# Optimization experiments

Measured on AMD Instinct MI355X. Metric: run time of the kernel, lower is better.

## Reference

```python
import jax, jax.numpy as jnp
import numpy as np

D = 768          # embedding_dim
H = 8            # attention heads
DH = D // H
HID = 512        # hidden_dim
N_LAYERS = 3     # graph conv layers
N_ETYPES = 5
LN_EPS = 1e-5


def setup_inputs() -> dict:
    key = jax.random.key(0)
    ks = jax.random.split(key, 32)
    N, E = 4096, 131072
    s = lambda fan: 1.0 / np.sqrt(fan)
    inp = {
        'node_features': jax.random.normal(ks[0], (N, D), jnp.float32),
        'edge_indices': jax.random.randint(ks[1], (2, E), 0, N, jnp.int64),
        'edge_types': jax.random.randint(ks[2], (E,), 0, N_ETYPES, jnp.int64),
        'node_types': jax.random.randint(ks[3], (N,), 0, 3, jnp.int64),
        # embedding tables
        'statute_emb': jax.random.normal(ks[4], (1000, D), jnp.float32),
        'case_emb': jax.random.normal(ks[5], (5000, D), jnp.float32),
        'article_emb': jax.random.normal(ks[6], (2000, D), jnp.float32),
        # per-layer conv params (stacked over 3 layers)
        'conv_msg_W': jax.random.uniform(ks[7], (N_LAYERS, N_ETYPES, D, D), jnp.float32, -s(D), s(D)),
        'conv_msg_b': jax.random.uniform(ks[8], (N_LAYERS, N_ETYPES, D), jnp.float32, -s(D), s(D)),
        'conv_upd_W': jax.random.uniform(ks[9], (N_LAYERS, D, 2 * D), jnp.float32, -s(2 * D), s(2 * D)),
        'conv_upd_b': jax.random.uniform(ks[10], (N_LAYERS, D), jnp.float32, -s(2 * D), s(2 * D)),
        'conv_ln_g': jnp.ones((N_LAYERS, D), jnp.float32),
        'conv_ln_b': jnp.zeros((N_LAYERS, D), jnp.float32),
        # MultiheadAttention params
        'in_proj_W': jax.random.uniform(ks[11], (3 * D, D), jnp.float32, -s(D), s(D)),
        'in_proj_b': jnp.zeros((3 * D,), jnp.float32),
        'out_proj_W': jax.random.uniform(ks[12], (D, D), jnp.float32, -s(D), s(D)),
        'out_proj_b': jnp.zeros((D,), jnp.float32),
        # network analyzer MLP
        'an_W1': jax.random.uniform(ks[13], (HID, D), jnp.float32, -s(D), s(D)),
        'an_b1': jax.random.uniform(ks[14], (HID,), jnp.float32, -s(D), s(D)),
        'an_W2': jax.random.uniform(ks[15], (HID // 2, HID), jnp.float32, -s(HID), s(HID)),
        'an_b2': jax.random.uniform(ks[16], (HID // 2,), jnp.float32, -s(HID), s(HID)),
        'an_W3': jax.random.uniform(ks[17], (1, HID // 2), jnp.float32, -s(HID // 2), s(HID // 2)),
        'an_b3': jax.random.uniform(ks[18], (1,), jnp.float32, -s(HID // 2), s(HID // 2)),
    }
    return inp


def _layer_norm(h, g, b):
    mu = h.mean(-1, keepdims=True)
    var = ((h - mu) ** 2).mean(-1, keepdims=True)
    return g * (h - mu) / jnp.sqrt(var + LN_EPS) + b


def _conv_layer(x, msg_W, msg_b, upd_W, upd_b, ln_g, ln_b, src, tgt, etypes):
    # x: [N, D]; src/tgt: [E]; etypes: [E]
    src_feats = x[src]                               # gather [E, D]
    agg = jnp.zeros_like(x)
    for t in range(N_ETYPES):                        # small fixed loop over edge types
        mask = (etypes == t)[:, None]
        msgs = jnp.where(mask, src_feats @ msg_W[t].T + msg_b[t], 0.0)
        agg = agg + jax.ops.segment_sum(msgs, tgt, num_segments=x.shape[0])
    combined = jnp.concatenate([x, agg], axis=-1)    # [N, 2D]
    upd = jax.nn.relu(combined @ upd_W.T + upd_b)    # dropout is identity in eval
    return _layer_norm(x + upd, ln_g, ln_b)


def reference(node_features, edge_indices, edge_types, node_types,
              statute_emb, case_emb, article_emb,
              conv_msg_W, conv_msg_b, conv_upd_W, conv_upd_b, conv_ln_g, conv_ln_b,
              in_proj_W, in_proj_b, out_proj_W, out_proj_b,
              an_W1, an_b1, an_W2, an_b2, an_W3, an_b3):
    N = node_features.shape[0]
    idx = jnp.arange(N)
    # per-node-type embedding lookup (i % table_size), vectorized
    emb = jnp.where((node_types == 0)[:, None], statute_emb[idx % 1000],
          jnp.where((node_types == 1)[:, None], case_emb[idx % 5000],
                    article_emb[idx % 2000]))
    x = node_features + emb

    src, tgt = edge_indices[0], edge_indices[1]
    for l in range(N_LAYERS):
        x = _conv_layer(x, conv_msg_W[l], conv_msg_b[l], conv_upd_W[l], conv_upd_b[l],
                        conv_ln_g[l], conv_ln_b[l], src, tgt, edge_types)

    # self-attention over all nodes (batch of 1), torch MHA semantics, eval mode
    qkv = x @ in_proj_W.T + in_proj_b                # [N, 3D]
    q, k, v = jnp.split(qkv, 3, axis=-1)
    to_h = lambda t: t.reshape(N, H, DH).transpose(1, 0, 2)   # [H, N, DH]
    q, k, v = to_h(q), to_h(k), to_h(v)
    scores = jnp.einsum('hqd,hkd->hqk', q, k) / jnp.sqrt(jnp.float32(DH))
    attn = jax.nn.softmax(scores, axis=-1)           # [H, N, N]
    ctx = jnp.einsum('hqk,hkd->hqd', attn, v).transpose(1, 0, 2).reshape(N, D)
    graph_repr = ctx @ out_proj_W.T + out_proj_b     # [N, D]
    attn_weights = attn.mean(0)                      # averaged over heads [N, N]

    pooled = graph_repr.mean(axis=0)                 # [D]
    h = jax.nn.relu(pooled @ an_W1.T + an_b1)
    h = jax.nn.relu(h @ an_W2.T + an_b2)
    network_score = jax.nn.sigmoid(h @ an_W3.T + an_b3)

    return x, graph_repr, network_score, attn_weights
```

## Files before the change

### kernel.cpp

```cpp
#include <hip/hip_runtime.h>

typedef unsigned short u16;
typedef unsigned int u32;
typedef __attribute__((ext_vector_type(4))) float f32x4;
typedef __attribute__((ext_vector_type(8))) __bf16 bf16x8;
typedef __attribute__((ext_vector_type(4))) unsigned int u32x4;

#define DEV static __device__ __forceinline__

#define NNODE 4096
#define DMODEL 768
#define NEDGE 131072

static constexpr size_t OFF_X     = 0;
static constexpr size_t OFF_X2    = 12582912;
static constexpr size_t OFF_AMSG  = 25165824;
static constexpr size_t OFF_AUPD  = 31457280;
static constexpr size_t OFF_WMSG  = 44040192;
static constexpr size_t OFF_WUPD  = 61734912;
static constexpr size_t OFF_WIP   = 68812800;
static constexpr size_t OFF_WOP   = 72351744;
static constexpr size_t OFF_Q     = 73531392;
static constexpr size_t OFF_K     = 79822848;
static constexpr size_t OFF_V     = 86114304;
static constexpr size_t OFF_CTX   = 92405760;
static constexpr size_t OFF_STATS = 98697216;
static constexpr size_t OFF_ML    = 98959360;
static constexpr size_t OFF_DEG   = 100007936;
static constexpr size_t OFF_OFFS  = 100024320;
static constexpr size_t OFF_CUR   = 100040960;
static constexpr size_t OFF_PACK  = 100057344;
static constexpr size_t OFF_PART  = 100581632;
static constexpr size_t OFF_POOL  = 100778240;
static constexpr size_t OFF_H1    = 100781312;
static constexpr size_t OFF_H2    = 100783360;
static constexpr size_t WS_TOTAL  = 100784384;

__device__ __attribute__((aligned(256))) unsigned char g_ws[WS_TOTAL];

DEV u16 f2bf(float f) {
  return __builtin_bit_cast(u16, (__bf16)f);
}
DEV void gl_lds16(const void* g, void* l) {
  __builtin_amdgcn_global_load_lds((const __attribute__((address_space(1))) void*)g,
                                   (__attribute__((address_space(3))) void*)l, 16, 0, 0);
}
DEV f32x4 mfma16(bf16x8 a, bf16x8 b, f32x4 c) {
  return __builtin_amdgcn_mfma_f32_16x16x32_bf16(a, b, c, 0, 0, 0);
}

__global__ void zero_kernel(int* p, int n) {
  int i = blockIdx.x * 256 + threadIdx.x;
  if (i < n) p[i] = 0;
}
__global__ void deg_kernel(const int* __restrict__ ei, int* __restrict__ deg) {
  int e = blockIdx.x * 256 + threadIdx.x;
  atomicAdd(&deg[ei[NEDGE + e]], 1);
}
__global__ void scan_kernel(const int* __restrict__ deg, int* __restrict__ offs, int* __restrict__ cur) {
  __shared__ int buf[1024];
  int t = threadIdx.x;
  int v0 = deg[t*4], v1 = deg[t*4+1], v2 = deg[t*4+2], v3 = deg[t*4+3];
  int s = v0 + v1 + v2 + v3;
  buf[t] = s;
  __syncthreads();
  for (int off = 1; off < 1024; off <<= 1) {
    int add = (t >= off) ? buf[t - off] : 0;
    __syncthreads();
    buf[t] += add;
    __syncthreads();
  }
  int run = buf[t] - s;
  offs[t*4] = run; cur[t*4] = run; run += v0;
  offs[t*4+1] = run; cur[t*4+1] = run; run += v1;
  offs[t*4+2] = run; cur[t*4+2] = run; run += v2;
  offs[t*4+3] = run; cur[t*4+3] = run; run += v3;
  if (t == 1023) offs[4096] = run;
}
__global__ void scatter_kernel(const int* __restrict__ ei, const int* __restrict__ ety,
                               int* __restrict__ cur, int* __restrict__ pack) {
  int e = blockIdx.x * 256 + threadIdx.x;
  int tg = ei[NEDGE + e];
  int pos = atomicAdd(&cur[tg], 1);
  pack[pos] = ei[e] | (ety[e] << 12);
}

__global__ void convert_bf_kernel(const float* __restrict__ W, u16* __restrict__ out, int total) {
  for (int i = blockIdx.x * 256 + threadIdx.x; i < total; i += gridDim.x * 256)
    out[i] = f2bf(W[i]);
}

__global__ void embed_kernel(const float* __restrict__ nf, const int* __restrict__ nty,
                             const float* __restrict__ se, const float* __restrict__ ce,
                             const float* __restrict__ ae,
                             float* __restrict__ x, u16* __restrict__ Amsg, u16* __restrict__ Aupd) {
  int v = blockIdx.x, t = threadIdx.x;
  int typ = nty[v];
  const float* tab = (typ == 0) ? se + (size_t)(v % 1000) * 768
                   : (typ == 1) ? ce + (size_t)(v % 5000) * 768
                                : ae + (size_t)(v % 2000) * 768;
  #pragma unroll
  for (int i = 0; i < 3; ++i) {
    int c = t + i * 256;
    float f = nf[(size_t)v * 768 + c] + tab[c];
    x[(size_t)v * 768 + c] = f;
    u16 hi = f2bf(f);
    Amsg[(size_t)v * 768 + c] = hi;
    Aupd[(size_t)v * 1536 + c] = hi;
  }
}

template<int EPI>
__global__ void __launch_bounds__(256, 3)
gemm_bt(const u16* __restrict__ A, int lda,
        const u16* __restrict__ B0, int ldb, int K,
        const float* __restrict__ bias0,
        float* __restrict__ C0, int ldc,
        const float* __restrict__ resid,
        u16* __restrict__ oq, u16* __restrict__ okk, u16* __restrict__ ov,
        long zsB, int zsBias, long zsC)
{
  __shared__ alignas(16) u16 sA[8192];
  __shared__ alignas(16) u16 sB[8192];
  const int tid = threadIdx.x;
  const int lane = tid & 63, wid = tid >> 6;
  const int wr = wid >> 1, wc = wid & 1;
  const int li = lane & 15, g = lane >> 4;
  const int bm = blockIdx.y * 128, bn = blockIdx.x * 128;
  const int z = blockIdx.z;
  const u16* B = B0 + (size_t)z * zsB;
  const float* bias = bias0 + (size_t)z * zsBias;

  const int srow = tid >> 3;
  const int scol = ((tid & 7) ^ (srow & 7)) * 8;
  const u16* Ag = A + (size_t)(bm + srow) * lda + scol;
  const u16* Bg = B + (size_t)(bn + srow) * ldb + scol;
  char* sAw = (char*)sA + wid * 1024;
  char* sBw = (char*)sB + wid * 1024;

  f32x4 acc[4][4];
  const f32x4 vz = {0.f, 0.f, 0.f, 0.f};
  #pragma unroll
  for (int i = 0; i < 4; ++i)
    #pragma unroll
    for (int j = 0; j < 4; ++j) acc[i][j] = vz;

  for (int k0 = 0; k0 < K; k0 += 64) {
    __syncthreads();
    #pragma unroll
    for (int is = 0; is < 4; ++is) {
      gl_lds16(Ag + (size_t)is * 32 * lda + k0, sAw + is * 4096);
      gl_lds16(Bg + (size_t)is * 32 * ldb + k0, sBw + is * 4096);
    }
    __syncthreads();
    #pragma unroll
    for (int kc = 0; kc < 2; ++kc) {
      bf16x8 av[4], bv[4];
      #pragma unroll
      for (int mt = 0; mt < 4; ++mt) {
        int row = wr * 64 + mt * 16 + li;
        av[mt] = *(const bf16x8*)((const char*)sA + row * 128 + ((kc * 64 + g * 16) ^ ((row & 7) << 4)));
      }
      #pragma unroll
      for (int nt = 0; nt < 4; ++nt) {
        int row = wc * 64 + nt * 16 + li;
        bv[nt] = *(const bf16x8*)((const char*)sB + row * 128 + ((kc * 64 + g * 16) ^ ((row & 7) << 4)));
      }
      #pragma unroll
      for (int mt = 0; mt < 4; ++mt)
        #pragma unroll
        for (int nt = 0; nt < 4; ++nt)
          acc[mt][nt] = mfma16(av[mt], bv[nt], acc[mt][nt]);
    }
  }
  #pragma unroll
  for (int mt = 0; mt < 4; ++mt) {
    #pragma unroll
    for (int nt = 0; nt < 4; ++nt) {
      #pragma unroll
      for (int r = 0; r < 4; ++r) {
        int gr = bm + wr * 64 + mt * 16 + g * 4 + r;
        int gc = bn + wc * 64 + nt * 16 + li;
        float v = acc[mt][nt][r] + bias[gc];
        if (EPI == 0) {
          C0[(size_t)z * zsC + (size_t)gr * ldc + gc] = v;
        } else if (EPI == 1) {
          C0[(size_t)gr * ldc + gc] = fmaxf(v, 0.f) + resid[(size_t)gr * 768 + gc];
        } else {
          int part = gc / 768;
          int j = gc - part * 768;
          int h = j / 96, d = j - h * 96;
          if (part == 0)      oq[((size_t)(h << 12) + gr) * 96 + d] = f2bf(v * (float)(0.10206207261596575 * 1.4426950408889634));
          else if (part == 1) okk[((size_t)(h << 12) + gr) * 96 + d] = f2bf(v);
          else                ov[((size_t)h * 96 + d) * 4096 + gr] = f2bf(v);
        }
      }
    }
  }
}

__global__ void agg_kernel(const float* __restrict__ Y, const int* __restrict__ offs,
                           const int* __restrict__ pack, u16* __restrict__ Aupd) {
  const int v = blockIdx.x, t = threadIdx.x;
  float a0 = 0.f, a1 = 0.f, a2 = 0.f;
  const int beg = offs[v], end = offs[v + 1];
  for (int i = beg; i < end; ++i) {
    int p = pack[i];
    const float* row = Y + (size_t)p * 768;
    a0 += row[t]; a1 += row[t + 256]; a2 += row[t + 512];
  }
  size_t b = (size_t)v * 1536 + 768;
  Aupd[b + t] = f2bf(a0); Aupd[b + t + 256] = f2bf(a1); Aupd[b + t + 512] = f2bf(a2);
}

__global__ void ln_kernel(const float* __restrict__ xin, const float* __restrict__ gam,
                          const float* __restrict__ bet,
                          float* __restrict__ x, u16* __restrict__ Amsg, u16* __restrict__ Aupd,
                          float* __restrict__ xcopy) {
  __shared__ float red[256];
  int v = blockIdx.x, t = threadIdx.x;
  const float* r = xin + (size_t)v * 768;
  float v0 = r[t], v1 = r[t + 256], v2 = r[t + 512];
  red[t] = v0 + v1 + v2;
  __syncthreads();
  for (int off = 128; off > 0; off >>= 1) { if (t < off) red[t] += red[t + off]; __syncthreads(); }
  float mu = red[0] * (1.f / 768.f);
  __syncthreads();
  float d0 = v0 - mu, d1 = v1 - mu, d2 = v2 - mu;
  red[t] = d0 * d0 + d1 * d1 + d2 * d2;
  __syncthreads();
  for (int off = 128; off > 0; off >>= 1) { if (t < off) red[t] += red[t + off]; __syncthreads(); }
  float rstd = rsqrtf(red[0] * (1.f / 768.f) + 1e-5f);
  float dv[3] = {d0, d1, d2};
  #pragma unroll
  for (int i = 0; i < 3; ++i) {
    int c = t + i * 256;
    float y = gam[c] * dv[i] * rstd + bet[c];
    x[(size_t)v * 768 + c] = y;
    if (xcopy) xcopy[(size_t)v * 768 + c] = y;
    u16 hi = f2bf(y);
    Amsg[(size_t)v * 768 + c] = hi;
    Aupd[(size_t)v * 1536 + c] = hi;
  }
}

__global__ void __launch_bounds__(256, 3)
flash_kernel(const u16* __restrict__ Qb, const u16* __restrict__ Kb,
             const u16* __restrict__ Vtb, float* __restrict__ Op,
             float* __restrict__ Mp, float* __restrict__ Lp) {
  __shared__ alignas(16) u16 sK[6144];
  __shared__ alignas(16) u16 sV[6144];
  __shared__ alignas(16) u16 sP[4][2048];
  const int tid = threadIdx.x, lane = tid & 63, wid = tid >> 6;
  const int li = lane & 15, g = lane >> 4;
  const int qt = blockIdx.x, h = blockIdx.y, kcb = blockIdx.z;
  const int vrow = tid >> 3, vcol = (tid & 7) ^ (vrow & 7);

  const u16* Qg = Qb + ((size_t)(h << 12) + qt * 128 + wid * 32 + li) * 96 + g * 8;
  bf16x8 aq0[3], aq1[3];
  #pragma unroll
  for (int kc = 0; kc < 3; ++kc) {
    aq0[kc] = *(const bf16x8*)(Qg + kc * 32);
    aq1[kc] = *(const bf16x8*)(Qg + 1536 + kc * 32);
  }

  float m0 = -1e30f, l0 = 0.f, m1 = -1e30f, l1 = 0.f;
  const f32x4 vz = {0.f, 0.f, 0.f, 0.f};
  f32x4 o0[6], o1[6];
  #pragma unroll
  for (int dt = 0; dt < 6; ++dt) { o0[dt] = vz; o1[dt] = vz; }

  const char* Kg = (const char*)(Kb + (size_t)(h << 12) * 96);
  const char* Vg = (const char*)(Vtb + (size_t)h * 96 * 4096);
  char* sKb = (char*)sK; char* sVb = (char*)sV; char* sPb = (char*)sP[wid];

  for (int kt = kcb * 16; kt < kcb * 16 + 16; ++kt) {
    __syncthreads();
    #pragma unroll
    for (int j = 0; j < 3; ++j) {
      gl_lds16(Kg + ((size_t)(kt * 64 + lane) * 96 + j * 32 + wid * 8) * 2, sKb + j * 4096 + wid * 1024);
      gl_lds16(Vg + (size_t)(j * 32 + vrow) * 8192 + kt * 128 + vcol * 16, sVb + j * 4096 + wid * 1024);
    }
    __syncthreads();

    f32x4 s0[4], s1[4];
    __builtin_amdgcn_s_setprio(1);
    #pragma unroll
    for (int nt = 0; nt < 4; ++nt) {
      s0[nt] = vz; s1[nt] = vz;
      #pragma unroll
      for (int kc = 0; kc < 3; ++kc) {
        bf16x8 bk = *(const bf16x8*)(sKb + kc * 4096 + g * 1024 + (nt * 16 + li) * 16);
        s0[nt] = mfma16(bk, aq0[kc], s0[nt]);
        s1[nt] = mfma16(bk, aq1[kc], s1[nt]);
      }
    }
    __builtin_amdgcn_s_setprio(0);

    {
      float mx = fmaxf(fmaxf(fmaxf(s0[0][0], s0[0][1]), fmaxf(s0[0][2], s0[0][3])),
                       fmaxf(fmaxf(s0[1][0], s0[1][1]), fmaxf(s0[1][2], s0[1][3])));
      mx = fmaxf(mx, fmaxf(fmaxf(fmaxf(s0[2][0], s0[2][1]), fmaxf(s0[2][2], s0[2][3])),
                           fmaxf(fmaxf(s0[3][0], s0[3][1]), fmaxf(s0[3][2], s0[3][3]))));
      mx = fmaxf(mx, __shfl_xor(mx, 16));
      mx = fmaxf(mx, __shfl_xor(mx, 32));
      if (__any(mx > m0 + 8.f)) {
        float mnew = fmaxf(m0, mx);
        float alpha = exp2f(m0 - mnew);
        l0 *= alpha;
        #pragma unroll
        for (int dt = 0; dt < 6; ++dt) o0[dt] *= alpha;
        m0 = mnew;
      }
      float rs = 0.f;
      #pragma unroll
      for (int nt = 0; nt < 4; ++nt)
        #pragma unroll
        for (int r = 0; r < 4; ++r) { float p = exp2f(s0[nt][r] - m0); s0[nt][r] = p; rs += p; }
      rs += __shfl_xor(rs, 16);
      rs += __shfl_xor(rs, 32);
      l0 += rs;
      #pragma unroll
      for (int nt = 0; nt < 4; ++nt)
        #pragma unroll
        for (int r0 = 0; r0 < 4; r0 += 2) {
          u32 w = (u32)f2bf(s0[nt][r0]) | ((u32)f2bf(s0[nt][r0 + 1]) << 16);
          *(u32*)(sPb + li * 128 + (((nt * 16 + g * 4 + r0) * 2) ^ ((li & 7) << 4))) = w;
        }
    }
    {
      float mx = fmaxf(fmaxf(fmaxf(s1[0][0], s1[0][1]), fmaxf(s1[0][2], s1[0][3])),
                       fmaxf(fmaxf(s1[1][0], s1[1][1]), fmaxf(s1[1][2], s1[1][3])));
      mx = fmaxf(mx, fmaxf(fmaxf(fmaxf(s1[2][0], s1[2][1]), fmaxf(s1[2][2], s1[2][3])),
                           fmaxf(fmaxf(s1[3][0], s1[3][1]), fmaxf(s1[3][2], s1[3][3]))));
      mx = fmaxf(mx, __shfl_xor(mx, 16));
      mx = fmaxf(mx, __shfl_xor(mx, 32));
      if (__any(mx > m1 + 8.f)) {
        float mnew = fmaxf(m1, mx);
        float alpha = exp2f(m1 - mnew);
        l1 *= alpha;
        #pragma unroll
        for (int dt = 0; dt < 6; ++dt) o1[dt] *= alpha;
        m1 = mnew;
      }
      float rs = 0.f;
      #pragma unroll
      for (int nt = 0; nt < 4; ++nt)
        #pragma unroll
        for (int r = 0; r < 4; ++r) { float p = exp2f(s1[nt][r] - m1); s1[nt][r] = p; rs += p; }
      rs += __shfl_xor(rs, 16);
      rs += __shfl_xor(rs, 32);
      l1 += rs;
      #pragma unroll
      for (int nt = 0; nt < 4; ++nt)
        #pragma unroll
        for (int r0 = 0; r0 < 4; r0 += 2) {
          u32 w = (u32)f2bf(s1[nt][r0]) | ((u32)f2bf(s1[nt][r0 + 1]) << 16);
          *(u32*)(sPb + (16 + li) * 128 + (((nt * 16 + g * 4 + r0) * 2) ^ ((li & 7) << 4))) = w;
        }
    }

    __builtin_amdgcn_s_setprio(1);
    #pragma unroll
    for (int kc2 = 0; kc2 < 2; ++kc2) {
      bf16x8 pa0 = *(const bf16x8*)(sPb + li * 128 + ((kc2 * 64 + g * 16) ^ ((li & 7) << 4)));
      bf16x8 pa1 = *(const bf16x8*)(sPb + (16 + li) * 128 + ((kc2 * 64 + g * 16) ^ ((li & 7) << 4)));
      #pragma unroll
      for (int dt = 0; dt < 6; ++dt) {
        int d = dt * 16 + li;
        bf16x8 bvv = *(const bf16x8*)(sVb + d * 128 + ((kc2 * 64 + g * 16) ^ ((d & 7) << 4)));
        o0[dt] = mfma16(pa0, bvv, o0[dt]);
        o1[dt] = mfma16(pa1, bvv, o1[dt]);
      }
    }
    __builtin_amdgcn_s_setprio(0);
  }
  int bq = qt * 128 + wid * 32;
  size_t cb = (size_t)(((kcb * 8 + h) << 12));
  #pragma unroll
  for (int dt = 0; dt < 6; ++dt)
    #pragma unroll
    for (int r = 0; r < 4; ++r) {
      int d = dt * 16 + li;
      Op[(cb + bq + g * 4 + r) * 96 + d] = o0[dt][r];
      Op[(cb + bq + 16 + g * 4 + r) * 96 + d] = o1[dt][r];
    }
  if (g == 0) {
    Mp[cb + bq + li] = m0;      Lp[cb + bq + li] = l0;
    Mp[cb + bq + 16 + li] = m1; Lp[cb + bq + 16 + li] = l1;
  }
}

__global__ void merge_kernel(const float* __restrict__ Op, const float* __restrict__ Mp,
                             const float* __restrict__ Lp,
                             u16* __restrict__ ctxb, float* __restrict__ stats) {
  int row = blockIdx.x, t = threadIdx.x;
  #pragma unroll
  for (int i = 0; i < 3; ++i) {
    int idx = t + i * 256;
    int h = idx / 96, d = idx - h * 96;
    int base = (h << 12) + row;
    float m0 = Mp[base], m1 = Mp[32768 + base], m2 = Mp[65536 + base], m3 = Mp[98304 + base];
    float M = fmaxf(fmaxf(m0, m1), fmaxf(m2, m3));
    float w0 = exp2f(m0 - M), w1 = exp2f(m1 - M), w2 = exp2f(m2 - M), w3 = exp2f(m3 - M);
    float L = w0 * Lp[base] + w1 * Lp[32768 + base] + w2 * Lp[65536 + base] + w3 * Lp[98304 + base];
    float o = w0 * Op[(size_t)base * 96 + d]
            + w1 * Op[(size_t)(32768 + base) * 96 + d]
            + w2 * Op[(size_t)(65536 + base) * 96 + d]
            + w3 * Op[(size_t)(98304 + base) * 96 + d];
    float invl = 1.f / L;
    ctxb[(size_t)row * 768 + idx] = f2bf(o * invl);
    if (d == 0) {
      stats[base] = M;
      stats[32768 + base] = invl;
    }
  }
}

__global__ void __launch_bounds__(256, 3)
mean_kernel(const u16* __restrict__ Qb, const u16* __restrict__ Kb,
            const float* __restrict__ stats, float* __restrict__ out) {
  __shared__ alignas(16) u16 sQ[12288];
  __shared__ alignas(16) u16 sK2[6144];
  const int tid = threadIdx.x, lane = tid & 63, wid = tid >> 6;
  const int li = lane & 15, g = lane >> 4;
  const int q0 = blockIdx.x * 128, k0 = blockIdx.y * 64;
  const f32x4 vz = {0.f, 0.f, 0.f, 0.f};
  f32x4 macc0[4], macc1[4];
  #pragma unroll
  for (int nt = 0; nt < 4; ++nt) { macc0[nt] = vz; macc1[nt] = vz; }
  char* sQb = (char*)sQ; char* sKb = (char*)sK2;
  const int rq = (wid & 1) * 64 + lane;
  const int ccb = wid >> 1;

  for (int h = 0; h < 8; ++h) {
    __syncthreads();
    #pragma unroll
    for (int i = 0; i < 6; ++i) {
      int cc = i * 2 + ccb, kc = cc >> 2, gg = cc & 3;
      gl_lds16((const char*)Qb + ((size_t)(h << 12) + q0 + rq) * 192 + kc * 64 + gg * 16,
               sQb + kc * 8192 + gg * 2048 + (wid & 1) * 1024);
    }
    #pragma unroll
    for (int i = 0; i < 3; ++i) {
      int c = i * 4 + wid, kc = c >> 2, gg = c & 3;
      gl_lds16((const char*)Kb + ((size_t)(h << 12) + k0 + lane) * 192 + kc * 64 + gg * 16,
               sKb + kc * 4096 + gg * 1024);
    }
    __syncthreads();

    bf16x8 a20[3], a21[3];
    #pragma unroll
    for (int kc = 0; kc < 3; ++kc) {
      a20[kc] = *(const bf16x8*)(sQb + kc * 8192 + g * 2048 + (wid * 32 + li) * 16);
      a21[kc] = *(const bf16x8*)(sQb + kc * 8192 + g * 2048 + (wid * 32 + 16 + li) * 16);
    }
    f32x4 s0[4], s1[4];
    __builtin_amdgcn_s_setprio(1);
    #pragma unroll
    for (int nt = 0; nt < 4; ++nt) {
      s0[nt] = vz; s1[nt] = vz;
      #pragma unroll
      for (int kc = 0; kc < 3; ++kc) {
        bf16x8 bk = *(const bf16x8*)(sKb + kc * 4096 + g * 1024 + (nt * 16 + li) * 16);
        s0[nt] = mfma16(a20[kc], bk, s0[nt]);
        s1[nt] = mfma16(a21[kc], bk, s1[nt]);
      }
    }
    __builtin_amdgcn_s_setprio(0);
    #pragma unroll
    for (int r = 0; r < 4; ++r) {
      int row0 = q0 + wid * 32 + g * 4 + r;
      float mm0 = stats[(h << 12) + row0];
      float si0 = 0.125f * stats[32768 + (h << 12) + row0];
      int row1 = row0 + 16;
      float mm1 = stats[(h << 12) + row1];
      float si1 = 0.125f * stats[32768 + (h << 12) + row1];
      #pragma unroll
      for (int nt = 0; nt < 4; ++nt) {
        macc0[nt][r] += exp2f(s0[nt][r] - mm0) * si0;
        macc1[nt][r] += exp2f(s1[nt][r] - mm1) * si1;
      }
    }
  }
  #pragma unroll
  for (int nt = 0; nt < 4; ++nt)
    #pragma unroll
    for (int r = 0; r < 4; ++r) {
      out[(size_t)(q0 + wid * 32 + g * 4 + r) * 4096 + k0 + nt * 16 + li] = macc0[nt][r];
      out[(size_t)(q0 + wid * 32 + 16 + g * 4 + r) * 4096 + k0 + nt * 16 + li] = macc1[nt][r];
    }
}

__global__ void colsum_kernel(const float* __restrict__ gr, float* __restrict__ part) {
  int b = blockIdx.x, t = threadIdx.x;
  float s0 = 0.f, s1 = 0.f, s2 = 0.f;
  for (int rr = 0; rr < 64; ++rr) {
    const float* row = gr + (size_t)(b * 64 + rr) * 768;
    s0 += row[t]; s1 += row[t + 256]; s2 += row[t + 512];
  }
  part[b * 768 + t] = s0; part[b * 768 + t + 256] = s1; part[b * 768 + t + 512] = s2;
}
__global__ void pool_kernel(const float* __restrict__ part, float* __restrict__ pool) {
  int t = blockIdx.x * 256 + threadIdx.x;
  float s = 0.f;
  #pragma unroll 8
  for (int b = 0; b < 64; ++b) s += part[b * 768 + t];
  pool[t] = s * (1.f / 4096.f);
}
template<int KDIM>
__global__ void mlp_fc_kernel(const float* __restrict__ in, const float* __restrict__ Wm,
                              const float* __restrict__ bb, float* __restrict__ outv) {
  int o = blockIdx.x * 4 + (threadIdx.x >> 6);
  int lane = threadIdx.x & 63;
  const float* w = Wm + (size_t)o * KDIM;
  float s = 0.f;
  #pragma unroll
  for (int k = lane; k < KDIM; k += 64) s += w[k] * in[k];
  s += __shfl_xor(s, 1);  s += __shfl_xor(s, 2);  s += __shfl_xor(s, 4);
  s += __shfl_xor(s, 8);  s += __shfl_xor(s, 16); s += __shfl_xor(s, 32);
  if (lane == 0) outv[o] = fmaxf(s + bb[o], 0.f);
}
__global__ void mlp3_kernel(const float* __restrict__ h2,
                            const float* __restrict__ W3, const float* __restrict__ b3,
                            float* __restrict__ out) {
  __shared__ float red[256];
  int t = threadIdx.x;
  red[t] = W3[t] * h2[t];
  __syncthreads();
  for (int off = 128; off > 0; off >>= 1) { if (t < off) red[t] += red[t + off]; __syncthreads(); }
  if (t == 0) out[0] = 1.f / (1.f + __expf(-(red[0] + b3[0])));
}

extern "C" void kernel_launch(void* const* d_in, const int* in_sizes, int n_in,
                              void* d_out, int out_size, void* d_ws, size_t ws_size,
                              hipStream_t stream) {
  const float* nf   = (const float*)d_in[0];
  const int*   ei   = (const int*)d_in[1];
  const int*   ety  = (const int*)d_in[2];
  const int*   nty  = (const int*)d_in[3];
  const float* se   = (const float*)d_in[4];
  const float* ce   = (const float*)d_in[5];
  const float* ae   = (const float*)d_in[6];
  const float* msgW = (const float*)d_in[7];
  const float* msgb = (const float*)d_in[8];
  const float* updW = (const float*)d_in[9];
  const float* updb = (const float*)d_in[10];
  const float* lng  = (const float*)d_in[11];
  const float* lnb  = (const float*)d_in[12];
  const float* ipW  = (const float*)d_in[13];
  const float* ipb  = (const float*)d_in[14];
  const float* opW  = (const float*)d_in[15];
  const float* opb  = (const float*)d_in[16];
  const float* aW1  = (const float*)d_in[17];
  const float* ab1  = (const float*)d_in[18];
  const float* aW2  = (const float*)d_in[19];
  const float* ab2  = (const float*)d_in[20];
  const float* aW3  = (const float*)d_in[21];
  const float* ab3  = (const float*)d_in[22];

  void* wsp = nullptr;
  hipGetSymbolAddress(&wsp, HIP_SYMBOL(g_ws));
  unsigned char* W = (unsigned char*)wsp;

  float* x     = (float*)(W + OFF_X);
  float* x2    = (float*)(W + OFF_X2);
  u16* Amsg    = (u16*)(W + OFF_AMSG);
  u16* Aupd    = (u16*)(W + OFF_AUPD);
  u16* Wmsg    = (u16*)(W + OFF_WMSG);
  u16* Wupd    = (u16*)(W + OFF_WUPD);
  u16* Wip     = (u16*)(W + OFF_WIP);
  u16* Wop     = (u16*)(W + OFF_WOP);
  u16* Qb      = (u16*)(W + OFF_Q);
  u16* Kb      = (u16*)(W + OFF_K);
  u16* Vtb     = (u16*)(W + OFF_V);
  u16* Ctxb    = (u16*)(W + OFF_CTX);
  float* stats = (float*)(W + OFF_STATS);
  float* Mp    = (float*)(W + OFF_ML);
  float* Lp    = Mp + 131072;
  int* deg     = (int*)(W + OFF_DEG);
  int* offs    = (int*)(W + OFF_OFFS);
  int* cur     = (int*)(W + OFF_CUR);
  int* pack    = (int*)(W + OFF_PACK);
  float* part  = (float*)(W + OFF_PART);
  float* pool  = (float*)(W + OFF_POOL);
  float* h1b   = (float*)(W + OFF_H1);
  float* h2b   = (float*)(W + OFF_H2);

  float* out_x    = (float*)d_out;
  float* out_gr   = out_x + (size_t)NNODE * DMODEL;
  float* out_sc   = out_gr + (size_t)NNODE * DMODEL;
  float* out_attn = out_sc + 1;
  float* Y        = out_attn;
  float* Op       = out_attn;

  zero_kernel<<<16, 256, 0, stream>>>(deg, NNODE);
  deg_kernel<<<NEDGE / 256, 256, 0, stream>>>(ei, deg);
  scan_kernel<<<1, 1024, 0, stream>>>(deg, offs, cur);
  scatter_kernel<<<NEDGE / 256, 256, 0, stream>>>(ei, ety, cur, pack);

  convert_bf_kernel<<<2048, 256, 0, stream>>>(msgW, Wmsg, 3 * 5 * 768 * 768);
  convert_bf_kernel<<<1024, 256, 0, stream>>>(updW, Wupd, 3 * 768 * 1536);
  convert_bf_kernel<<<1024, 256, 0, stream>>>(ipW, Wip, 2304 * 768);
  convert_bf_kernel<<<512, 256, 0, stream>>>(opW, Wop, 768 * 768);

  embed_kernel<<<NNODE, 256, 0, stream>>>(nf, nty, se, ce, ae, x, Amsg, Aupd);

  for (int l = 0; l < 3; ++l) {
    gemm_bt<0><<<dim3(6, 32, 5), 256, 0, stream>>>(Amsg, 768,
        Wmsg + (size_t)l * 5 * 768 * 768, 768, 768,
        msgb + (size_t)l * 5 * 768, Y, 768, nullptr, nullptr, nullptr, nullptr,
        (long)768 * 768, 768, (long)NNODE * DMODEL);
    agg_kernel<<<NNODE, 256, 0, stream>>>(Y, offs, pack, Aupd);
    gemm_bt<1><<<dim3(6, 32, 1), 256, 0, stream>>>(Aupd, 1536,
        Wupd + (size_t)l * 768 * 1536, 1536, 1536,
        updb + (size_t)l * 768, x2, 768, x, nullptr, nullptr, nullptr, 0, 0, 0);
    ln_kernel<<<NNODE, 256, 0, stream>>>(x2, lng + (size_t)l * 768, lnb + (size_t)l * 768,
        x, Amsg, Aupd, (l == 2) ? out_x : nullptr);
  }

  gemm_bt<2><<<dim3(18, 32, 1), 256, 0, stream>>>(Amsg, 768, Wip, 768, 768,
      ipb, nullptr, 0, nullptr, Qb, Kb, Vtb, 0, 0, 0);
  flash_kernel<<<dim3(32, 8, 4), 256, 0, stream>>>(Qb, Kb, Vtb, Op, Mp, Lp);
  merge_kernel<<<NNODE, 256, 0, stream>>>(Op, Mp, Lp, Ctxb, stats);
  mean_kernel<<<dim3(32, 64), 256, 0, stream>>>(Qb, Kb, stats, out_attn);
  gemm_bt<0><<<dim3(6, 32, 1), 256, 0, stream>>>(Ctxb, 768, Wop, 768, 768,
      opb, out_gr, 768, nullptr, nullptr, nullptr, nullptr, 0, 0, 0);

  colsum_kernel<<<64, 256, 0, stream>>>(out_gr, part);
  pool_kernel<<<3, 256, 0, stream>>>(part, pool);
  mlp_fc_kernel<768><<<128, 256, 0, stream>>>(pool, aW1, ab1, h1b);
  mlp_fc_kernel<512><<<64, 256, 0, stream>>>(h1b, aW2, ab2, h2b);
  mlp3_kernel<<<1, 256, 0, stream>>>(h2b, aW3, ab3, out_sc);
}
```

Baseline: 741.1 us.

## Load K/V fragments directly into registers with double-buffered K prefetch in flash kernel

Removes the shared-memory staging of K and V tiles and the two block-wide barriers per tile in the flash attention kernel. Each wave now loads its MFMA operand fragments for K and V straight from global memory into registers, and prefetches the next tile's K while the softmax runs, alternating between two register buffers. Launch bounds drop from 3 to 2 waves per SIMD to make room for the extra registers. In exchange, each wave loads K/V redundantly instead of sharing via LDS, so global/L2 traffic rises and occupancy falls.

```diff
diff --git a/kernel.cpp b/kernel.cpp
--- a/kernel.cpp
+++ b/kernel.cpp
@@ -244,17 +244,29 @@
   }
 }
 
-__global__ void __launch_bounds__(256, 3)
+DEV void kload(bf16x8* kk, const u16* Kg, int row0, int li, int g) {
+  #pragma unroll
+  for (int nt = 0; nt < 4; ++nt)
+    #pragma unroll
+    for (int kc = 0; kc < 3; ++kc)
+      kk[nt * 3 + kc] = *(const bf16x8*)(Kg + (size_t)(row0 + nt * 16 + li) * 96 + kc * 32 + g * 8);
+}
+DEV void vload(bf16x8* vv, const u16* Vg, int col0, int li, int g) {
+  #pragma unroll
+  for (int dt = 0; dt < 6; ++dt)
+    #pragma unroll
+    for (int kc2 = 0; kc2 < 2; ++kc2)
+      vv[dt * 2 + kc2] = *(const bf16x8*)(Vg + (size_t)(dt * 16 + li) * 4096 + col0 + kc2 * 32 + g * 8);
+}
+
+__global__ void __launch_bounds__(256, 2)
 flash_kernel(const u16* __restrict__ Qb, const u16* __restrict__ Kb,
              const u16* __restrict__ Vtb, float* __restrict__ Op,
              float* __restrict__ Mp, float* __restrict__ Lp) {
-  __shared__ alignas(16) u16 sK[6144];
-  __shared__ alignas(16) u16 sV[6144];
   __shared__ alignas(16) u16 sP[4][2048];
   const int tid = threadIdx.x, lane = tid & 63, wid = tid >> 6;
   const int li = lane & 15, g = lane >> 4;
   const int qt = blockIdx.x, h = blockIdx.y, kcb = blockIdx.z;
-  const int vrow = tid >> 3, vcol = (tid & 7) ^ (vrow & 7);
 
   const u16* Qg = Qb + ((size_t)(h << 12) + qt * 128 + wid * 32 + li) * 96 + g * 8;
   bf16x8 aq0[3], aq1[3];
@@ -270,111 +282,113 @@
   #pragma unroll
   for (int dt = 0; dt < 6; ++dt) { o0[dt] = vz; o1[dt] = vz; }
 
-  const char* Kg = (const char*)(Kb + (size_t)(h << 12) * 96);
-  const char* Vg = (const char*)(Vtb + (size_t)h * 96 * 4096);
-  char* sKb = (char*)sK; char* sVb = (char*)sV; char* sPb = (char*)sP[wid];
-
-  for (int kt = kcb * 16; kt < kcb * 16 + 16; ++kt) {
-    __syncthreads();
-    #pragma unroll
-    for (int j = 0; j < 3; ++j) {
-      gl_lds16(Kg + ((size_t)(kt * 64 + lane) * 96 + j * 32 + wid * 8) * 2, sKb + j * 4096 + wid * 1024);
-      gl_lds16(Vg + (size_t)(j * 32 + vrow) * 8192 + kt * 128 + vcol * 16, sVb + j * 4096 + wid * 1024);
-    }
-    __syncthreads();
-
-    f32x4 s0[4], s1[4];
-    __builtin_amdgcn_s_setprio(1);
-    #pragma unroll
-    for (int nt = 0; nt < 4; ++nt) {
-      s0[nt] = vz; s1[nt] = vz;
-      #pragma unroll
-      for (int kc = 0; kc < 3; ++kc) {
-        bf16x8 bk = *(const bf16x8*)(sKb + kc * 4096 + g * 1024 + (nt * 16 + li) * 16);
-        s0[nt] = mfma16(bk, aq0[kc], s0[nt]);
-        s1[nt] = mfma16(bk, aq1[kc], s1[nt]);
-      }
-    }
-    __builtin_amdgcn_s_setprio(0);
-
-    {
-      float mx = fmaxf(fmaxf(fmaxf(s0[0][0], s0[0][1]), fmaxf(s0[0][2], s0[0][3])),
-                       fmaxf(fmaxf(s0[1][0], s0[1][1]), fmaxf(s0[1][2], s0[1][3])));
-      mx = fmaxf(mx, fmaxf(fmaxf(fmaxf(s0[2][0], s0[2][1]), fmaxf(s0[2][2], s0[2][3])),
-                           fmaxf(fmaxf(s0[3][0], s0[3][1]), fmaxf(s0[3][2], s0[3][3]))));
-      mx = fmaxf(mx, __shfl_xor(mx, 16));
-      mx = fmaxf(mx, __shfl_xor(mx, 32));
-      if (__any(mx > m0 + 8.f)) {
-        float mnew = fmaxf(m0, mx);
-        float alpha = exp2f(m0 - mnew);
-        l0 *= alpha;
-        #pragma unroll
-        for (int dt = 0; dt < 6; ++dt) o0[dt] *= alpha;
-        m0 = mnew;
-      }
-      float rs = 0.f;
-      #pragma unroll
-      for (int nt = 0; nt < 4; ++nt)
-        #pragma unroll
-        for (int r = 0; r < 4; ++r) { float p = exp2f(s0[nt][r] - m0); s0[nt][r] = p; rs += p; }
-      rs += __shfl_xor(rs, 16);
-      rs += __shfl_xor(rs, 32);
-      l0 += rs;
-      #pragma unroll
-      for (int nt = 0; nt < 4; ++nt)
-        #pragma unroll
-        for (int r0 = 0; r0 < 4; r0 += 2) {
-          u32 w = (u32)f2bf(s0[nt][r0]) | ((u32)f2bf(s0[nt][r0 + 1]) << 16);
-          *(u32*)(sPb + li * 128 + (((nt * 16 + g * 4 + r0) * 2) ^ ((li & 7) << 4))) = w;
-        }
-    }
-    {
-      float mx = fmaxf(fmaxf(fmaxf(s1[0][0], s1[0][1]), fmaxf(s1[0][2], s1[0][3])),
-                       fmaxf(fmaxf(s1[1][0], s1[1][1]), fmaxf(s1[1][2], s1[1][3])));
-      mx = fmaxf(mx, fmaxf(fmaxf(fmaxf(s1[2][0], s1[2][1]), fmaxf(s1[2][2], s1[2][3])),
-                           fmaxf(fmaxf(s1[3][0], s1[3][1]), fmaxf(s1[3][2], s1[3][3]))));
-      mx = fmaxf(mx, __shfl_xor(mx, 16));
-      mx = fmaxf(mx, __shfl_xor(mx, 32));
-      if (__any(mx > m1 + 8.f)) {
-        float mnew = fmaxf(m1, mx);
-        float alpha = exp2f(m1 - mnew);
-        l1 *= alpha;
-        #pragma unroll
-        for (int dt = 0; dt < 6; ++dt) o1[dt] *= alpha;
-        m1 = mnew;
-      }
-      float rs = 0.f;
-      #pragma unroll
-      for (int nt = 0; nt < 4; ++nt)
-        #pragma unroll
-        for (int r = 0; r < 4; ++r) { float p = exp2f(s1[nt][r] - m1); s1[nt][r] = p; rs += p; }
-      rs += __shfl_xor(rs, 16);
-      rs += __shfl_xor(rs, 32);
-      l1 += rs;
-      #pragma unroll
-      for (int nt = 0; nt < 4; ++nt)
-        #pragma unroll
-        for (int r0 = 0; r0 < 4; r0 += 2) {
-          u32 w = (u32)f2bf(s1[nt][r0]) | ((u32)f2bf(s1[nt][r0 + 1]) << 16);
-          *(u32*)(sPb + (16 + li) * 128 + (((nt * 16 + g * 4 + r0) * 2) ^ ((li & 7) << 4))) = w;
-        }
-    }
-
-    __builtin_amdgcn_s_setprio(1);
-    #pragma unroll
-    for (int kc2 = 0; kc2 < 2; ++kc2) {
-      bf16x8 pa0 = *(const bf16x8*)(sPb + li * 128 + ((kc2 * 64 + g * 16) ^ ((li & 7) << 4)));
-      bf16x8 pa1 = *(const bf16x8*)(sPb + (16 + li) * 128 + ((kc2 * 64 + g * 16) ^ ((li & 7) << 4)));
-      #pragma unroll
-      for (int dt = 0; dt < 6; ++dt) {
-        int d = dt * 16 + li;
-        bf16x8 bvv = *(const bf16x8*)(sVb + d * 128 + ((kc2 * 64 + g * 16) ^ ((d & 7) << 4)));
-        o0[dt] = mfma16(pa0, bvv, o0[dt]);
-        o1[dt] = mfma16(pa1, bvv, o1[dt]);
-      }
-    }
-    __builtin_amdgcn_s_setprio(0);
-  }
+  const u16* Kg = Kb + (size_t)(h << 12) * 96;
+  const u16* Vg = Vtb + (size_t)h * 96 * 4096;
+  char* sPb = (char*)sP[wid];
+
+  const int kst = kcb * 16, kend = kst + 16;
+  bf16x8 ka[12], kb2[12], vv[12];
+  kload(ka, Kg, kst * 64, li, g);
+
+#define FLASH_TILE(KT, KIN, KOUT)                                                        \
+  {                                                                                      \
+    const int ktc = (KT);                                                                \
+    f32x4 s0[4], s1[4];                                                                  \
+    __builtin_amdgcn_s_setprio(1);                                                       \
+    _Pragma("unroll")                                                                    \
+    for (int nt = 0; nt < 4; ++nt) {                                                     \
+      s0[nt] = vz; s1[nt] = vz;                                                          \
+      _Pragma("unroll")                                                                  \
+      for (int kc = 0; kc < 3; ++kc) {                                                   \
+        s0[nt] = mfma16(KIN[nt * 3 + kc], aq0[kc], s0[nt]);                              \
+        s1[nt] = mfma16(KIN[nt * 3 + kc], aq1[kc], s1[nt]);                              \
+      }                                                                                  \
+    }                                                                                    \
+    __builtin_amdgcn_s_setprio(0);                                                       \
+    vload(vv, Vg, ktc * 64, li, g);                                                      \
+    if (ktc + 1 < kend) kload(KOUT, Kg, (ktc + 1) * 64, li, g);                          \
+    {                                                                                    \
+      float mx = fmaxf(fmaxf(fmaxf(s0[0][0], s0[0][1]), fmaxf(s0[0][2], s0[0][3])),     \
+                       fmaxf(fmaxf(s0[1][0], s0[1][1]), fmaxf(s0[1][2], s0[1][3])));    \
+      mx = fmaxf(mx, fmaxf(fmaxf(fmaxf(s0[2][0], s0[2][1]), fmaxf(s0[2][2], s0[2][3])), \
+                           fmaxf(fmaxf(s0[3][0], s0[3][1]), fmaxf(s0[3][2], s0[3][3])))); \
+      mx = fmaxf(mx, __shfl_xor(mx, 16));                                                \
+      mx = fmaxf(mx, __shfl_xor(mx, 32));                                                \
+      if (__any(mx > m0 + 8.f)) {                                                        \
+        float mnew = fmaxf(m0, mx);                                                      \
+        float alpha = exp2f(m0 - mnew);                                                  \
+        l0 *= alpha;                                                                     \
+        _Pragma("unroll")                                                                \
+        for (int dt = 0; dt < 6; ++dt) o0[dt] *= alpha;                                  \
+        m0 = mnew;                                                                       \
+      }                                                                                  \
+      float rs = 0.f;                                                                    \
+      _Pragma("unroll")                                                                  \
+      for (int nt = 0; nt < 4; ++nt)                                                     \
+        _Pragma("unroll")                                                                \
+        for (int r = 0; r < 4; ++r) { float p = exp2f(s0[nt][r] - m0); s0[nt][r] = p; rs += p; } \
+      rs += __shfl_xor(rs, 16);                                                          \
+      rs += __shfl_xor(rs, 32);                                                          \
+      l0 += rs;                                                                          \
+      _Pragma("unroll")                                                                  \
+      for (int nt = 0; nt < 4; ++nt)                                                     \
+        _Pragma("unroll")                                                                \
+        for (int r0 = 0; r0 < 4; r0 += 2) {                                              \
+          u32 w = (u32)f2bf(s0[nt][r0]) | ((u32)f2bf(s0[nt][r0 + 1]) << 16);             \
+          *(u32*)(sPb + li * 128 + (((nt * 16 + g * 4 + r0) * 2) ^ ((li & 7) << 4))) = w; \
+        }                                                                                \
+    }                                                                                    \
+    {                                                                                    \
+      float mx = fmaxf(fmaxf(fmaxf(s1[0][0], s1[0][1]), fmaxf(s1[0][2], s1[0][3])),     \
+                       fmaxf(fmaxf(s1[1][0], s1[1][1]), fmaxf(s1[1][2], s1[1][3])));    \
+      mx = fmaxf(mx, fmaxf(fmaxf(fmaxf(s1[2][0], s1[2][1]), fmaxf(s1[2][2], s1[2][3])), \
+                           fmaxf(fmaxf(s1[3][0], s1[3][1]), fmaxf(s1[3][2], s1[3][3])))); \
+      mx = fmaxf(mx, __shfl_xor(mx, 16));                                                \
+      mx = fmaxf(mx, __shfl_xor(mx, 32));                                                \
+      if (__any(mx > m1 + 8.f)) {                                                        \
+        float mnew = fmaxf(m1, mx);                                                      \
+        float alpha = exp2f(m1 - mnew);                                                  \
+        l1 *= alpha;                                                                     \
+        _Pragma("unroll")                                                                \
+        for (int dt = 0; dt < 6; ++dt) o1[dt] *= alpha;                                  \
+        m1 = mnew;                                                                       \
+      }                                                                                  \
+      float rs = 0.f;                                                                    \
+      _Pragma("unroll")                                                                  \
+      for (int nt = 0; nt < 4; ++nt)                                                     \
+        _Pragma("unroll")                                                                \
+        for (int r = 0; r < 4; ++r) { float p = exp2f(s1[nt][r] - m1); s1[nt][r] = p; rs += p; } \
+      rs += __shfl_xor(rs, 16);                                                          \
+      rs += __shfl_xor(rs, 32);                                                          \
+      l1 += rs;                                                                          \
+      _Pragma("unroll")                                                                  \
+      for (int nt = 0; nt < 4; ++nt)                                                     \
+        _Pragma("unroll")                                                                \
+        for (int r0 = 0; r0 < 4; r0 += 2) {                                              \
+          u32 w = (u32)f2bf(s1[nt][r0]) | ((u32)f2bf(s1[nt][r0 + 1]) << 16);             \
+          *(u32*)(sPb + (16 + li) * 128 + (((nt * 16 + g * 4 + r0) * 2) ^ ((li & 7) << 4))) = w; \
+        }                                                                                \
+    }                                                                                    \
+    __builtin_amdgcn_s_setprio(1);                                                       \
+    _Pragma("unroll")                                                                    \
+    for (int kc2 = 0; kc2 < 2; ++kc2) {                                                  \
+      bf16x8 pa0 = *(const bf16x8*)(sPb + li * 128 + ((kc2 * 64 + g * 16) ^ ((li & 7) << 4)));        \
+      bf16x8 pa1 = *(const bf16x8*)(sPb + (16 + li) * 128 + ((kc2 * 64 + g * 16) ^ ((li & 7) << 4))); \
+      _Pragma("unroll")                                                                  \
+      for (int dt = 0; dt < 6; ++dt) {                                                   \
+        o0[dt] = mfma16(pa0, vv[dt * 2 + kc2], o0[dt]);                                  \
+        o1[dt] = mfma16(pa1, vv[dt * 2 + kc2], o1[dt]);                                  \
+      }                                                                                  \
+    }                                                                                    \
+    __builtin_amdgcn_s_setprio(0);                                                       \
+  }
+
+  for (int kt = kst; kt < kend; kt += 2) {
+    FLASH_TILE(kt, ka, kb2);
+    FLASH_TILE(kt + 1, kb2, ka);
+  }
+#undef FLASH_TILE
+
   int bq = qt * 128 + wid * 32;
   size_t cb = (size_t)(((kcb * 8 + h) << 12));
   #pragma unroll
```

New measurement: 846.4 us. +14.2%, slower.

## Store per-edge-type message outputs in bf16 and simplify flash softmax rescaling

Applied to the files above, without the earlier changes.

The message GEMM now writes its per-edge-type outputs as bf16 through a new epilogue, and the aggregation kernel reads those bf16 rows and converts them to float. This roughly halves the bytes written by the GEMM and the bytes gathered during aggregation, at some cost in precision. The flash-attention kernel also drops its lazy rescale (which skipped rescaling unless the max grew by more than 8) and now rescales every tile. The Q pre-scale loses its log2(e) factor, and the exp2f calls in the flash, merge and mean kernels become __expf, so every tile now pays for the rescale multiplies on the output accumulators.

```diff
diff --git a/kernel.cpp b/kernel.cpp
--- a/kernel.cpp
+++ b/kernel.cpp
@@ -41,6 +41,10 @@
 DEV u16 f2bf(float f) {
   return __builtin_bit_cast(u16, (__bf16)f);
 }
+DEV float bf2f(u16 h) {
+  union { unsigned u; float f; } v; v.u = ((unsigned)h) << 16;
+  return v.f;
+}
 DEV void gl_lds16(const void* g, void* l) {
   __builtin_amdgcn_global_load_lds((const __attribute__((address_space(1))) void*)g,
                                    (__attribute__((address_space(3))) void*)l, 16, 0, 0);
@@ -186,11 +190,13 @@
           C0[(size_t)z * zsC + (size_t)gr * ldc + gc] = v;
         } else if (EPI == 1) {
           C0[(size_t)gr * ldc + gc] = fmaxf(v, 0.f) + resid[(size_t)gr * 768 + gc];
+        } else if (EPI == 3) {
+          oq[(size_t)z * zsC + (size_t)gr * ldc + gc] = f2bf(v);
         } else {
           int part = gc / 768;
           int j = gc - part * 768;
           int h = j / 96, d = j - h * 96;
-          if (part == 0)      oq[((size_t)(h << 12) + gr) * 96 + d] = f2bf(v * (float)(0.10206207261596575 * 1.4426950408889634));
+          if (part == 0)      oq[((size_t)(h << 12) + gr) * 96 + d] = f2bf(v * 0.10206207261596575f);
           else if (part == 1) okk[((size_t)(h << 12) + gr) * 96 + d] = f2bf(v);
           else                ov[((size_t)h * 96 + d) * 4096 + gr] = f2bf(v);
         }
@@ -199,15 +205,15 @@
   }
 }
 
-__global__ void agg_kernel(const float* __restrict__ Y, const int* __restrict__ offs,
+__global__ void agg_kernel(const u16* __restrict__ Y, const int* __restrict__ offs,
                            const int* __restrict__ pack, u16* __restrict__ Aupd) {
   const int v = blockIdx.x, t = threadIdx.x;
   float a0 = 0.f, a1 = 0.f, a2 = 0.f;
   const int beg = offs[v], end = offs[v + 1];
   for (int i = beg; i < end; ++i) {
     int p = pack[i];
-    const float* row = Y + (size_t)p * 768;
-    a0 += row[t]; a1 += row[t + 256]; a2 += row[t + 512];
+    const u16* row = Y + (size_t)p * 768;
+    a0 += bf2f(row[t]); a1 += bf2f(row[t + 256]); a2 += bf2f(row[t + 512]);
   }
   size_t b = (size_t)v * 1536 + 768;
   Aupd[b + t] = f2bf(a0); Aupd[b + t + 256] = f2bf(a1); Aupd[b + t + 512] = f2bf(a2);
@@ -304,22 +310,19 @@
                            fmaxf(fmaxf(s0[3][0], s0[3][1]), fmaxf(s0[3][2], s0[3][3]))));
       mx = fmaxf(mx, __shfl_xor(mx, 16));
       mx = fmaxf(mx, __shfl_xor(mx, 32));
-      if (__any(mx > m0 + 8.f)) {
-        float mnew = fmaxf(m0, mx);
-        float alpha = exp2f(m0 - mnew);
-        l0 *= alpha;
-        #pragma unroll
-        for (int dt = 0; dt < 6; ++dt) o0[dt] *= alpha;
-        m0 = mnew;
-      }
+      float mnew = fmaxf(m0, mx);
+      float alpha = __expf(m0 - mnew);
       float rs = 0.f;
       #pragma unroll
       for (int nt = 0; nt < 4; ++nt)
         #pragma unroll
-        for (int r = 0; r < 4; ++r) { float p = exp2f(s0[nt][r] - m0); s0[nt][r] = p; rs += p; }
+        for (int r = 0; r < 4; ++r) { float p = __expf(s0[nt][r] - mnew); s0[nt][r] = p; rs += p; }
       rs += __shfl_xor(rs, 16);
       rs += __shfl_xor(rs, 32);
-      l0 += rs;
+      l0 = l0 * alpha + rs;
+      m0 = mnew;
+      #pragma unroll
+      for (int dt = 0; dt < 6; ++dt) o0[dt] *= alpha;
       #pragma unroll
       for (int nt = 0; nt < 4; ++nt)
         #pragma unroll
@@ -335,22 +338,19 @@
                            fmaxf(fmaxf(s1[3][0], s1[3][1]), fmaxf(s1[3][2], s1[3][3]))));
       mx = fmaxf(mx, __shfl_xor(mx, 16));
       mx = fmaxf(mx, __shfl_xor(mx, 32));
-      if (__any(mx > m1 + 8.f)) {
-        float mnew = fmaxf(m1, mx);
-        float alpha = exp2f(m1 - mnew);
-        l1 *= alpha;
-        #pragma unroll
-        for (int dt = 0; dt < 6; ++dt) o1[dt] *= alpha;
-        m1 = mnew;
-      }
+      float mnew = fmaxf(m1, mx);
+      float alpha = __expf(m1 - mnew);
       float rs = 0.f;
       #pragma unroll
       for (int nt = 0; nt < 4; ++nt)
         #pragma unroll
-        for (int r = 0; r < 4; ++r) { float p = exp2f(s1[nt][r] - m1); s1[nt][r] = p; rs += p; }
+        for (int r = 0; r < 4; ++r) { float p = __expf(s1[nt][r] - mnew); s1[nt][r] = p; rs += p; }
       rs += __shfl_xor(rs, 16);
       rs += __shfl_xor(rs, 32);
-      l1 += rs;
+      l1 = l1 * alpha + rs;
+      m1 = mnew;
+      #pragma unroll
+      for (int dt = 0; dt < 6; ++dt) o1[dt] *= alpha;
       #pragma unroll
       for (int nt = 0; nt < 4; ++nt)
         #pragma unroll
@@ -402,7 +402,7 @@
     int base = (h << 12) + row;
     float m0 = Mp[base], m1 = Mp[32768 + base], m2 = Mp[65536 + base], m3 = Mp[98304 + base];
     float M = fmaxf(fmaxf(m0, m1), fmaxf(m2, m3));
-    float w0 = exp2f(m0 - M), w1 = exp2f(m1 - M), w2 = exp2f(m2 - M), w3 = exp2f(m3 - M);
+    float w0 = __expf(m0 - M), w1 = __expf(m1 - M), w2 = __expf(m2 - M), w3 = __expf(m3 - M);
     float L = w0 * Lp[base] + w1 * Lp[32768 + base] + w2 * Lp[65536 + base] + w3 * Lp[98304 + base];
     float o = w0 * Op[(size_t)base * 96 + d]
             + w1 * Op[(size_t)(32768 + base) * 96 + d]
@@ -478,8 +478,8 @@
       float si1 = 0.125f * stats[32768 + (h << 12) + row1];
       #pragma unroll
       for (int nt = 0; nt < 4; ++nt) {
-        macc0[nt][r] += exp2f(s0[nt][r] - mm0) * si0;
-        macc1[nt][r] += exp2f(s1[nt][r] - mm1) * si1;
+        macc0[nt][r] += __expf(s0[nt][r] - mm0) * si0;
+        macc1[nt][r] += __expf(s1[nt][r] - mm1) * si1;
       }
     }
   }
@@ -591,7 +591,7 @@
   float* out_gr   = out_x + (size_t)NNODE * DMODEL;
   float* out_sc   = out_gr + (size_t)NNODE * DMODEL;
   float* out_attn = out_sc + 1;
-  float* Y        = out_attn;
+  u16*   Yb       = (u16*)out_attn;
   float* Op       = out_attn;
 
   zero_kernel<<<16, 256, 0, stream>>>(deg, NNODE);
@@ -607,11 +607,11 @@
   embed_kernel<<<NNODE, 256, 0, stream>>>(nf, nty, se, ce, ae, x, Amsg, Aupd);
 
   for (int l = 0; l < 3; ++l) {
-    gemm_bt<0><<<dim3(6, 32, 5), 256, 0, stream>>>(Amsg, 768,
+    gemm_bt<3><<<dim3(6, 32, 5), 256, 0, stream>>>(Amsg, 768,
         Wmsg + (size_t)l * 5 * 768 * 768, 768, 768,
-        msgb + (size_t)l * 5 * 768, Y, 768, nullptr, nullptr, nullptr, nullptr,
+        msgb + (size_t)l * 5 * 768, nullptr, 768, nullptr, Yb, nullptr, nullptr,
         (long)768 * 768, 768, (long)NNODE * DMODEL);
-    agg_kernel<<<NNODE, 256, 0, stream>>>(Y, offs, pack, Aupd);
+    agg_kernel<<<NNODE, 256, 0, stream>>>(Yb, offs, pack, Aupd);
     gemm_bt<1><<<dim3(6, 32, 1), 256, 0, stream>>>(Aupd, 1536,
         Wupd + (size_t)l * 768 * 1536, 1536, 1536,
         updb + (size_t)l * 768, x2, 768, x, nullptr, nullptr, nullptr, 0, 0, 0);
```

After: 654.1 us. -11.7%, faster.
